# Kernel optimization log

Measured on AMD Instinct MI355X. Metric: run time of the kernel, lower is better.

The kernel has to match this reference:

```python
import jax, jax.numpy as jnp
import numpy as np

N, E, IN_DIM, OUT_DIM, H = 4096, 131072, 1024, 512, 4


def setup_inputs() -> dict:
    key = jax.random.key(0)
    k1, k2, k3, k4 = jax.random.split(key, 4)
    x = jax.random.normal(k1, (N, IN_DIM), dtype=jnp.float32)
    edge_index = jax.random.randint(k2, (2, E), 0, N, dtype=jnp.int64)
    # learned params, scaled like torch Linear init (~1/sqrt(fan_in))
    W = jax.random.normal(k3, (H, IN_DIM, OUT_DIM), dtype=jnp.float32) * 0.02
    a = jax.random.normal(k4, (H, 2 * OUT_DIM), dtype=jnp.float32) * 0.02
    return {"x": x, "edge_index": edge_index, "W": W, "a": a}


def reference(x, edge_index, W, a):
    row, col = edge_index[0], edge_index[1]
    n = x.shape[0]
    h = jnp.einsum('ni,hio->hno', x, W)                    # [H, N, out]
    # per-edge attention logits: a . [h[row] || h[col]]
    a_src, a_dst = a[:, :OUT_DIM], a[:, OUT_DIM:]
    e = (jnp.einsum('heo,ho->he', h[:, row], a_src)
         + jnp.einsum('heo,ho->he', h[:, col], a_dst))      # [H, E]
    e = jnp.where(e > 0, e, 0.2 * e)                        # LeakyReLU(0.2)
    # dense NxN attention matrix exactly as the original (zeros at non-edges
    # DO participate in the row softmax, matching the torch code)
    att = jnp.zeros((H, n, n), dtype=h.dtype).at[:, row, col].set(e)
    att = jax.nn.softmax(att, axis=-1)
    h_prime = jnp.einsum('hnm,hmo->hno', att, h)            # [H, N, out]
    return jnp.transpose(h_prime, (1, 0, 2)).reshape(n, H * OUT_DIM)
```

## Files before the change

### kernel.cpp

```cpp
#include <hip/hip_runtime.h>
#include <stdint.h>

#define NN 4096
#define EE 131072
#define IND 1024
#define OUTD 512
#define NH 4
#define NBKT 8
#define BKT_SHIFT 9

typedef __bf16 bf16x8 __attribute__((ext_vector_type(8)));
typedef float f32x4 __attribute__((ext_vector_type(4)));
typedef float f32x2 __attribute__((ext_vector_type(2)));

__device__ __forceinline__ unsigned short f2bf(float f) {
  unsigned u = __float_as_uint(f);
  u += 0x7FFFu + ((u >> 16) & 1u);
  return (unsigned short)(u >> 16);
}

__global__ void cast_x_kernel(const float* __restrict__ x, unsigned short* __restrict__ xb) {
  int i = blockIdx.x * 256 + threadIdx.x;
  float4 v = ((const float4*)x)[i];
  ushort4 o;
  o.x = f2bf(v.x); o.y = f2bf(v.y); o.z = f2bf(v.z); o.w = f2bf(v.w);
  ((ushort4*)xb)[i] = o;
}

__global__ void transpose_w_kernel(const float* __restrict__ W, unsigned short* __restrict__ Wt) {
  __shared__ float tile[32][33];
  int i0 = blockIdx.x * 32, o0 = blockIdx.y * 32, h = blockIdx.z;
  int tx = threadIdx.x, ty = threadIdx.y;
#pragma unroll
  for (int r = 0; r < 32; r += 8)
    tile[ty + r][tx] = W[((size_t)(h * IND + i0 + ty + r)) * OUTD + o0 + tx];
  __syncthreads();
#pragma unroll
  for (int r = 0; r < 32; r += 8)
    Wt[((size_t)(h * OUTD + o0 + ty + r)) * IND + i0 + tx] = f2bf(tile[tx][ty + r]);
}

__device__ __forceinline__ void gload16(const unsigned short* g, unsigned short* l) {
  __builtin_amdgcn_global_load_lds((const __attribute__((address_space(1))) void*)g,
                                   (__attribute__((address_space(3))) void*)l, 16, 0, 0);
}

__global__ __launch_bounds__(256, 2) void gemm_kernel(
    const unsigned short* __restrict__ X, const unsigned short* __restrict__ Wt,
    const float* __restrict__ Av, unsigned char* __restrict__ Hb8,
    float* __restrict__ s4_src, float* __restrict__ s4_dst, float* __restrict__ Scol) {
  __shared__ __align__(16) unsigned short As[2][4096];
  __shared__ __align__(16) unsigned short Bs[2][4096];
  const int t = threadIdx.x, w = t >> 6, lane = t & 63;
  const int bx = blockIdx.x, by = blockIdx.y, hh = blockIdx.z;

  const unsigned short* Ab0 = X + (size_t)(by * 128) * IND;
  const unsigned short* Bb0 = Wt + (size_t)(hh * OUTD + bx * 128) * IND;

  const int seg0 = w * 64 + lane, seg1 = (4 + w) * 64 + lane;
  const int r0 = seg0 >> 2, c0 = (seg0 & 3) ^ (r0 & 3);
  const int r1 = seg1 >> 2, c1 = (seg1 & 3) ^ (r1 & 3);

  const int wr = w >> 1, wc = w & 1, g = lane >> 4, rlo = lane & 15;
  int aoff[4], boff[4];
#pragma unroll
  for (int i = 0; i < 4; i++) {
    int ra = wr * 64 + i * 16 + rlo;
    aoff[i] = ra * 64 + ((g ^ (ra & 3)) << 4);
    int rb = wc * 64 + i * 16 + rlo;
    boff[i] = rb * 64 + ((g ^ (rb & 3)) << 4);
  }

  f32x4 zero = {0.f, 0.f, 0.f, 0.f};
  f32x4 acc[4][4];
#pragma unroll
  for (int i = 0; i < 4; i++)
#pragma unroll
    for (int j = 0; j < 4; j++) acc[i][j] = zero;

#define STAGE(buf, kt)                                                   \
  do {                                                                   \
    const unsigned short* ga = Ab0 + (kt) * 32;                          \
    const unsigned short* gb = Bb0 + (kt) * 32;                          \
    gload16(ga + r0 * IND + c0 * 8, &As[buf][w * 512]);                  \
    gload16(ga + r1 * IND + c1 * 8, &As[buf][(4 + w) * 512]);            \
    gload16(gb + r0 * IND + c0 * 8, &Bs[buf][w * 512]);                  \
    gload16(gb + r1 * IND + c1 * 8, &Bs[buf][(4 + w) * 512]);            \
  } while (0)

  STAGE(0, 0);
  __syncthreads();
  int cur = 0;
  for (int kt = 0; kt < 32; ++kt) {
    if (kt != 31) STAGE(cur ^ 1, kt + 1);
    const char* Abuf = (const char*)As[cur];
    const char* Bbuf = (const char*)Bs[cur];
    bf16x8 av[4], bv[4];
#pragma unroll
    for (int i = 0; i < 4; i++) {
      av[i] = *(const bf16x8*)(Abuf + aoff[i]);
      bv[i] = *(const bf16x8*)(Bbuf + boff[i]);
    }
#pragma unroll
    for (int i = 0; i < 4; i++)
#pragma unroll
      for (int j = 0; j < 4; j++)
        acc[i][j] = __builtin_amdgcn_mfma_f32_16x16x32_bf16(av[i], bv[j], acc[i][j], 0, 0, 0);
    __syncthreads();
    cur ^= 1;
  }
#undef STAGE

#pragma unroll
  for (int i = 0; i < 4; i++)
#pragma unroll
    for (int j = 0; j < 4; j++) {
      int mm0 = by * 128 + wr * 64 + i * 16 + g * 4;
      int nn = bx * 128 + wc * 64 + j * 16 + rlo;
#pragma unroll
      for (int q = 0; q < 4; q++) {
        int p = __builtin_amdgcn_cvt_pk_fp8_f32(acc[i][j][q], acc[i][j][q], 0, false);
        Hb8[((size_t)(mm0 + q) * NH + hh) * OUTD + nn] = (unsigned char)p;
      }
    }

  float as_[4], ad_[4];
#pragma unroll
  for (int j = 0; j < 4; j++) {
    int nn = bx * 128 + wc * 64 + j * 16 + rlo;
    as_[j] = Av[hh * 2 * OUTD + nn];
    ad_[j] = Av[hh * 2 * OUTD + OUTD + nn];
  }
#pragma unroll
  for (int i = 0; i < 4; i++)
#pragma unroll
    for (int q = 0; q < 4; q++) {
      float vs = 0.f, vd = 0.f;
#pragma unroll
      for (int j = 0; j < 4; j++) {
        float tv = acc[i][j][q];
        vs += tv * as_[j];
        vd += tv * ad_[j];
      }
#pragma unroll
      for (int m = 1; m < 16; m <<= 1) {
        vs += __shfl_xor(vs, m);
        vd += __shfl_xor(vd, m);
      }
      if (rlo == 0) {
        int r = by * 128 + wr * 64 + i * 16 + g * 4 + q;
        atomicAdd(&s4_src[r * NH + hh], vs);
        atomicAdd(&s4_dst[r * NH + hh], vd);
      }
    }

#pragma unroll
  for (int j = 0; j < 4; j++) {
    float cv = 0.f;
#pragma unroll
    for (int i = 0; i < 4; i++)
#pragma unroll
      for (int q = 0; q < 4; q++) cv += acc[i][j][q];
    cv += __shfl_xor(cv, 16);
    cv += __shfl_xor(cv, 32);
    if (g == 0) {
      int nn = bx * 128 + wc * 64 + j * 16 + rlo;
      atomicAdd(&Scol[hh * OUTD + nn], cv);
    }
  }
}

__global__ void edge_a_kernel(const int* __restrict__ ei, unsigned* __restrict__ bitmap,
                              int* __restrict__ counts2, unsigned char* __restrict__ flags) {
  int e = blockIdx.x * 256 + threadIdx.x;
  int row = ei[e], col = ei[EE + e];
  unsigned key = ((unsigned)row << 12) | (unsigned)col;
  unsigned bit = 1u << (key & 31);
  unsigned old = atomicOr(&bitmap[key >> 5], bit);
  if (old & bit) { flags[e] = 1; return; }
  flags[e] = 0;
  atomicAdd(&counts2[row * NBKT + (col >> BKT_SHIFT)], 1);
}

__global__ void scan_part_kernel(const int* __restrict__ counts2, int* __restrict__ bsum) {
  __shared__ int wsum[4];
  int b = blockIdx.x, t = threadIdx.x, w = t >> 6, lane = t & 63;
  int v = counts2[b * 256 + t];
#pragma unroll
  for (int d = 1; d < 64; d <<= 1) v += __shfl_xor(v, d);
  if (lane == 0) wsum[w] = v;
  __syncthreads();
  if (t == 0) bsum[b] = wsum[0] + wsum[1] + wsum[2] + wsum[3];
}

__global__ void scan_top_kernel(const int* __restrict__ bsum, int* __restrict__ bpre,
                                int* __restrict__ offsets2) {
  int t = threadIdx.x;
  int v0 = bsum[2 * t], v1 = bsum[2 * t + 1];
  int s = v0 + v1, inc = s;
#pragma unroll
  for (int d = 1; d < 64; d <<= 1) {
    int u = __shfl_up(inc, d);
    if (t >= d) inc += u;
  }
  int excl = inc - s;
  bpre[2 * t] = excl;
  bpre[2 * t + 1] = excl + v0;
  if (t == 63) offsets2[NN * NBKT] = inc;
}

__global__ void scan_down_kernel(const int* __restrict__ counts2, const int* __restrict__ bpre,
                                 int* __restrict__ offsets2, int* __restrict__ cursor2) {
  __shared__ int wsum[4];
  int b = blockIdx.x, t = threadIdx.x, w = t >> 6, lane = t & 63;
  int idx = b * 256 + t;
  int v = counts2[idx];
  int inc = v;
#pragma unroll
  for (int d = 1; d < 64; d <<= 1) {
    int u = __shfl_up(inc, d);
    if (lane >= d) inc += u;
  }
  if (lane == 63) wsum[w] = inc;
  __syncthreads();
  int wpre = 0;
#pragma unroll
  for (int k = 0; k < 4; k++)
    if (k < w) wpre += wsum[k];
  int excl = bpre[b] + wpre + inc - v;
  offsets2[idx] = excl;
  cursor2[idx] = excl;
}

__global__ void edge_b_kernel(const int* __restrict__ ei, const unsigned char* __restrict__ flags,
                              const float* __restrict__ s4_src, const float* __restrict__ s4_dst,
                              int* __restrict__ cursor2, int* __restrict__ csr_col,
                              float* __restrict__ csr_g4) {
  int e = blockIdx.x * 256 + threadIdx.x;
  if (flags[e]) return;
  int row = ei[e], col = ei[EE + e];
  int pos = atomicAdd(&cursor2[row * NBKT + (col >> BKT_SHIFT)], 1);
  csr_col[pos] = col;
  float4 ss = *(const float4*)(s4_src + row * NH);
  float4 sd = *(const float4*)(s4_dst + col * NH);
  float4 gv;
  float e0 = ss.x + sd.x; e0 = e0 > 0.f ? e0 : 0.2f * e0; gv.x = expf(e0) - 1.0f;
  float e1 = ss.y + sd.y; e1 = e1 > 0.f ? e1 : 0.2f * e1; gv.y = expf(e1) - 1.0f;
  float e2 = ss.z + sd.z; e2 = e2 > 0.f ? e2 : 0.2f * e2; gv.z = expf(e2) - 1.0f;
  float e3 = ss.w + sd.w; e3 = e3 > 0.f ? e3 : 0.2f * e3; gv.w = expf(e3) - 1.0f;
  *(float4*)(csr_g4 + (size_t)pos * NH) = gv;
}

__global__ __launch_bounds__(256) void finalize_kernel(
    const unsigned char* __restrict__ Hb8,
    const float* __restrict__ S, const int* __restrict__ offsets2,
    const int* __restrict__ csr_col, const float* __restrict__ csr_g4,
    float* __restrict__ out) {
  __shared__ int cols_s[64];
  __shared__ float g_s[4][64];
  const int i = blockIdx.x, t = threadIdx.x;
  const int w = t >> 6, lane = t & 63;

  float acc[8];
  {
    const float4* Sv = (const float4*)(S + w * OUTD + lane * 8);
    float4 s0 = Sv[0], s1 = Sv[1];
    acc[0] = s0.x; acc[1] = s0.y; acc[2] = s0.z; acc[3] = s0.w;
    acc[4] = s1.x; acc[5] = s1.y; acc[6] = s1.z; acc[7] = s1.w;
  }
  float gsum = 0.f;

  const int start = offsets2[i * NBKT];
  const int cnt = offsets2[(i + 1) * NBKT] - start;
  for (int base = 0; base < cnt; base += 64) {
    int nload = min(64, cnt - base);
    __syncthreads();
    if (w == 0) cols_s[lane] = (lane < nload) ? csr_col[start + base + lane] : 0;
    {
      int el = t >> 2;
      float gvv = (el < nload) ? csr_g4[(size_t)(start + base) * NH + t] : 0.f;
      g_s[t & 3][el] = gvv;
    }
    __syncthreads();
#pragma unroll 2
    for (int k = 0; k < nload; k++) {
      int cc = cols_s[k];
      float gg = g_s[w][k];
      gsum += gg;
      uint2 u = *(const uint2*)(Hb8 + ((size_t)(cc * NH + w)) * OUTD + lane * 8);
      f32x2 p0 = __builtin_amdgcn_cvt_pk_f32_fp8(u.x, false);
      f32x2 p1 = __builtin_amdgcn_cvt_pk_f32_fp8(u.x, true);
      f32x2 p2 = __builtin_amdgcn_cvt_pk_f32_fp8(u.y, false);
      f32x2 p3 = __builtin_amdgcn_cvt_pk_f32_fp8(u.y, true);
      acc[0] += gg * p0[0];
      acc[1] += gg * p0[1];
      acc[2] += gg * p1[0];
      acc[3] += gg * p1[1];
      acc[4] += gg * p2[0];
      acc[5] += gg * p2[1];
      acc[6] += gg * p3[0];
      acc[7] += gg * p3[1];
    }
  }

  float inv = 1.0f / ((float)NN + gsum);
  float4 o0, o1;
  o0.x = acc[0] * inv; o0.y = acc[1] * inv; o0.z = acc[2] * inv; o0.w = acc[3] * inv;
  o1.x = acc[4] * inv; o1.y = acc[5] * inv; o1.z = acc[6] * inv; o1.w = acc[7] * inv;
  float* ob = out + (size_t)i * (NH * OUTD) + w * OUTD + lane * 8;
  ((float4*)ob)[0] = o0;
  ((float4*)ob)[1] = o1;
}

extern "C" void kernel_launch(void* const* d_in, const int* in_sizes, int n_in,
                              void* d_out, int out_size, void* d_ws, size_t ws_size,
                              hipStream_t stream) {
  const float* x = (const float*)d_in[0];
  const int* ei = (const int*)d_in[1];
  const float* W = (const float*)d_in[2];
  const float* a = (const float*)d_in[3];
  float* out = (float*)d_out;

  char* ws = (char*)d_ws;
  unsigned short* xb = (unsigned short*)(ws);
  unsigned short* wt = (unsigned short*)(ws + (8ull << 20));
  unsigned char* Hb8 = (unsigned char*)(ws + (12ull << 20));
  char* scal = ws + (20ull << 20);
  float* s4_src = (float*)(scal);
  float* s4_dst = (float*)(scal + 65536);
  float* Scol = (float*)(scal + 2 * 65536);
  unsigned char* flags = (unsigned char*)(ws + (21ull << 20));
  unsigned* bitmap = (unsigned*)(ws + (22ull << 20));
  int* counts2 = (int*)(ws + (24ull << 20));
  int* offsets2 = (int*)(ws + (24ull << 20) + 262144);
  int* cursor2 = (int*)(ws + (24ull << 20) + 2 * 262144);
  int* bsum = (int*)(ws + (24ull << 20) + 3 * 262144);
  int* bpre = (int*)(ws + (24ull << 20) + 3 * 262144 + 1024);
  int* csr_col = (int*)(ws + (25ull << 20));
  float* csr_g4 = (float*)(ws + (26ull << 20));

  hipMemsetAsync(scal, 0, 2 * 65536 + 8192, stream);
  hipMemsetAsync(bitmap, 0, (size_t)NN * NN / 8, stream);
  hipMemsetAsync(counts2, 0, NN * NBKT * 4, stream);

  cast_x_kernel<<<4096, 256, 0, stream>>>(x, xb);
  transpose_w_kernel<<<dim3(32, 16, 4), dim3(32, 8), 0, stream>>>(W, wt);
  gemm_kernel<<<dim3(4, 32, 4), 256, 0, stream>>>(xb, wt, a, Hb8, s4_src, s4_dst, Scol);
  edge_a_kernel<<<EE / 256, 256, 0, stream>>>(ei, bitmap, counts2, flags);
  scan_part_kernel<<<128, 256, 0, stream>>>(counts2, bsum);
  scan_top_kernel<<<1, 64, 0, stream>>>(bsum, bpre, offsets2);
  scan_down_kernel<<<128, 256, 0, stream>>>(counts2, bpre, offsets2, cursor2);
  edge_b_kernel<<<EE / 256, 256, 0, stream>>>(ei, flags, s4_src, s4_dst, cursor2, csr_col,
                                              csr_g4);
  finalize_kernel<<<NN, 256, 0, stream>>>(Hb8, Scol, offsets2, csr_col, csr_g4, out);
}
```

Baseline: 184.1 us.

## Merge prep kernels, single-block scan, one memset, GEMM block swizzle, deeper unroll

Merges the x cast and W transpose into one launch and replaces the three-kernel scan with one 1024-thread block. The three memsets become one by placing the zeroed buffers next to each other. The GEMM grid is flattened into a 1D grid with a remapped block order to change how blocks land across XCDs and the cache, and the finalize inner loop is unrolled 4x instead of 2x. The main aim is fewer launches and less launch gap. The single-block scan runs serially over 32K counters, and the unroll may raise register pressure.

```diff
diff --git a/kernel.cpp b/kernel.cpp
--- a/kernel.cpp
+++ b/kernel.cpp
@@ -19,25 +19,28 @@
   return (unsigned short)(u >> 16);
 }
 
-__global__ void cast_x_kernel(const float* __restrict__ x, unsigned short* __restrict__ xb) {
-  int i = blockIdx.x * 256 + threadIdx.x;
-  float4 v = ((const float4*)x)[i];
-  ushort4 o;
-  o.x = f2bf(v.x); o.y = f2bf(v.y); o.z = f2bf(v.z); o.w = f2bf(v.w);
-  ((ushort4*)xb)[i] = o;
-}
-
-__global__ void transpose_w_kernel(const float* __restrict__ W, unsigned short* __restrict__ Wt) {
+__global__ void prep_kernel(const float* __restrict__ x, unsigned short* __restrict__ xb,
+                            const float* __restrict__ W, unsigned short* __restrict__ Wt) {
   __shared__ float tile[32][33];
-  int i0 = blockIdx.x * 32, o0 = blockIdx.y * 32, h = blockIdx.z;
-  int tx = threadIdx.x, ty = threadIdx.y;
-#pragma unroll
-  for (int r = 0; r < 32; r += 8)
-    tile[ty + r][tx] = W[((size_t)(h * IND + i0 + ty + r)) * OUTD + o0 + tx];
-  __syncthreads();
-#pragma unroll
-  for (int r = 0; r < 32; r += 8)
-    Wt[((size_t)(h * OUTD + o0 + ty + r)) * IND + i0 + tx] = f2bf(tile[tx][ty + r]);
+  const int bid = blockIdx.x, t = threadIdx.x;
+  if (bid < 4096) {
+    int i = bid * 256 + t;
+    float4 v = ((const float4*)x)[i];
+    ushort4 o;
+    o.x = f2bf(v.x); o.y = f2bf(v.y); o.z = f2bf(v.z); o.w = f2bf(v.w);
+    ((ushort4*)xb)[i] = o;
+  } else {
+    int b2 = bid - 4096;
+    int i0 = (b2 & 31) * 32, o0 = ((b2 >> 5) & 15) * 32, h = b2 >> 9;
+    int tx = t & 31, ty = t >> 5;
+#pragma unroll
+    for (int r = 0; r < 32; r += 8)
+      tile[ty + r][tx] = W[((size_t)(h * IND + i0 + ty + r)) * OUTD + o0 + tx];
+    __syncthreads();
+#pragma unroll
+    for (int r = 0; r < 32; r += 8)
+      Wt[((size_t)(h * OUTD + o0 + ty + r)) * IND + i0 + tx] = f2bf(tile[tx][ty + r]);
+  }
 }
 
 __device__ __forceinline__ void gload16(const unsigned short* g, unsigned short* l) {
@@ -52,7 +55,9 @@
   __shared__ __align__(16) unsigned short As[2][4096];
   __shared__ __align__(16) unsigned short Bs[2][4096];
   const int t = threadIdx.x, w = t >> 6, lane = t & 63;
-  const int bx = blockIdx.x, by = blockIdx.y, hh = blockIdx.z;
+  const int B = blockIdx.x;
+  const int L = ((B & 7) << 6) | (B >> 3);
+  const int bx = L & 3, hh = (L >> 2) & 3, by = L >> 4;
 
   const unsigned short* Ab0 = X + (size_t)(by * 128) * IND;
   const unsigned short* Bb0 = Wt + (size_t)(hh * OUTD + bx * 128) * IND;
@@ -182,54 +187,46 @@
   atomicAdd(&counts2[row * NBKT + (col >> BKT_SHIFT)], 1);
 }
 
-__global__ void scan_part_kernel(const int* __restrict__ counts2, int* __restrict__ bsum) {
-  __shared__ int wsum[4];
-  int b = blockIdx.x, t = threadIdx.x, w = t >> 6, lane = t & 63;
-  int v = counts2[b * 256 + t];
-#pragma unroll
-  for (int d = 1; d < 64; d <<= 1) v += __shfl_xor(v, d);
-  if (lane == 0) wsum[w] = v;
-  __syncthreads();
-  if (t == 0) bsum[b] = wsum[0] + wsum[1] + wsum[2] + wsum[3];
-}
-
-__global__ void scan_top_kernel(const int* __restrict__ bsum, int* __restrict__ bpre,
-                                int* __restrict__ offsets2) {
-  int t = threadIdx.x;
-  int v0 = bsum[2 * t], v1 = bsum[2 * t + 1];
-  int s = v0 + v1, inc = s;
-#pragma unroll
-  for (int d = 1; d < 64; d <<= 1) {
-    int u = __shfl_up(inc, d);
-    if (t >= d) inc += u;
-  }
-  int excl = inc - s;
-  bpre[2 * t] = excl;
-  bpre[2 * t + 1] = excl + v0;
-  if (t == 63) offsets2[NN * NBKT] = inc;
-}
-
-__global__ void scan_down_kernel(const int* __restrict__ counts2, const int* __restrict__ bpre,
-                                 int* __restrict__ offsets2, int* __restrict__ cursor2) {
-  __shared__ int wsum[4];
-  int b = blockIdx.x, t = threadIdx.x, w = t >> 6, lane = t & 63;
-  int idx = b * 256 + t;
-  int v = counts2[idx];
-  int inc = v;
+__global__ __launch_bounds__(1024) void scan_kernel(const int* __restrict__ c2,
+                                                    int* __restrict__ off2,
+                                                    int* __restrict__ cur2) {
+  __shared__ int wtot[16];
+  const int t = threadIdx.x, w = t >> 6, lane = t & 63;
+  int loc[32];
+  const int4* src = (const int4*)c2 + t * 8;
+#pragma unroll
+  for (int k = 0; k < 8; k++) {
+    int4 v = src[k];
+    loc[4 * k] = v.x; loc[4 * k + 1] = v.y; loc[4 * k + 2] = v.z; loc[4 * k + 3] = v.w;
+  }
+  int s = 0;
+#pragma unroll
+  for (int k = 0; k < 32; k++) s += loc[k];
+  int inc = s;
 #pragma unroll
   for (int d = 1; d < 64; d <<= 1) {
     int u = __shfl_up(inc, d);
     if (lane >= d) inc += u;
   }
-  if (lane == 63) wsum[w] = inc;
+  if (lane == 63) wtot[w] = inc;
   __syncthreads();
   int wpre = 0;
-#pragma unroll
-  for (int k = 0; k < 4; k++)
-    if (k < w) wpre += wsum[k];
-  int excl = bpre[b] + wpre + inc - v;
-  offsets2[idx] = excl;
-  cursor2[idx] = excl;
+  for (int k = 0; k < 16; k++)
+    if (k < w) wpre += wtot[k];
+  int o = wpre + inc - s;
+  if (t == 1023) off2[NN * NBKT] = o + s;
+  int4* od = (int4*)off2 + t * 8;
+  int4* cd = (int4*)cur2 + t * 8;
+#pragma unroll
+  for (int k = 0; k < 8; k++) {
+    int4 ov;
+    ov.x = o; o += loc[4 * k];
+    ov.y = o; o += loc[4 * k + 1];
+    ov.z = o; o += loc[4 * k + 2];
+    ov.w = o; o += loc[4 * k + 3];
+    od[k] = ov;
+    cd[k] = ov;
+  }
 }
 
 __global__ void edge_b_kernel(const int* __restrict__ ei, const unsigned char* __restrict__ flags,
@@ -282,7 +279,7 @@
       g_s[t & 3][el] = gvv;
     }
     __syncthreads();
-#pragma unroll 2
+#pragma unroll 4
     for (int k = 0; k < nload; k++) {
       int cc = cols_s[k];
       float gg = g_s[w][k];
@@ -325,31 +322,25 @@
   unsigned short* xb = (unsigned short*)(ws);
   unsigned short* wt = (unsigned short*)(ws + (8ull << 20));
   unsigned char* Hb8 = (unsigned char*)(ws + (12ull << 20));
-  char* scal = ws + (20ull << 20);
-  float* s4_src = (float*)(scal);
-  float* s4_dst = (float*)(scal + 65536);
-  float* Scol = (float*)(scal + 2 * 65536);
-  unsigned char* flags = (unsigned char*)(ws + (21ull << 20));
-  unsigned* bitmap = (unsigned*)(ws + (22ull << 20));
-  int* counts2 = (int*)(ws + (24ull << 20));
-  int* offsets2 = (int*)(ws + (24ull << 20) + 262144);
-  int* cursor2 = (int*)(ws + (24ull << 20) + 2 * 262144);
-  int* bsum = (int*)(ws + (24ull << 20) + 3 * 262144);
-  int* bpre = (int*)(ws + (24ull << 20) + 3 * 262144 + 1024);
-  int* csr_col = (int*)(ws + (25ull << 20));
-  float* csr_g4 = (float*)(ws + (26ull << 20));
-
-  hipMemsetAsync(scal, 0, 2 * 65536 + 8192, stream);
-  hipMemsetAsync(bitmap, 0, (size_t)NN * NN / 8, stream);
-  hipMemsetAsync(counts2, 0, NN * NBKT * 4, stream);
-
-  cast_x_kernel<<<4096, 256, 0, stream>>>(x, xb);
-  transpose_w_kernel<<<dim3(32, 16, 4), dim3(32, 8), 0, stream>>>(W, wt);
-  gemm_kernel<<<dim3(4, 32, 4), 256, 0, stream>>>(xb, wt, a, Hb8, s4_src, s4_dst, Scol);
+  char* zreg = ws + (20ull << 20);
+  float* s4_src = (float*)(zreg);
+  float* s4_dst = (float*)(zreg + 65536);
+  float* Scol = (float*)(zreg + 2 * 65536);
+  int* counts2 = (int*)(zreg + 2 * 65536 + 8192);
+  unsigned* bitmap = (unsigned*)(zreg + 2 * 65536 + 8192 + 131072);
+  const size_t ZBYTES = 2 * 65536 + 8192 + 131072 + ((size_t)NN * NN / 8);
+  unsigned char* flags = (unsigned char*)(ws + (23ull << 20));
+  int* offsets2 = (int*)(ws + (23ull << 20) + 262144);
+  int* cursor2 = (int*)(ws + (23ull << 20) + 2 * 262144);
+  int* csr_col = (int*)(ws + (24ull << 20));
+  float* csr_g4 = (float*)(ws + (25ull << 20));
+
+  hipMemsetAsync(zreg, 0, ZBYTES, stream);
+
+  prep_kernel<<<4096 + 2048, 256, 0, stream>>>(x, xb, W, wt);
+  gemm_kernel<<<512, 256, 0, stream>>>(xb, wt, a, Hb8, s4_src, s4_dst, Scol);
   edge_a_kernel<<<EE / 256, 256, 0, stream>>>(ei, bitmap, counts2, flags);
-  scan_part_kernel<<<128, 256, 0, stream>>>(counts2, bsum);
-  scan_top_kernel<<<1, 64, 0, stream>>>(bsum, bpre, offsets2);
-  scan_down_kernel<<<128, 256, 0, stream>>>(counts2, bpre, offsets2, cursor2);
+  scan_kernel<<<1, 1024, 0, stream>>>(counts2, offsets2, cursor2);
   edge_b_kernel<<<EE / 256, 256, 0, stream>>>(ei, flags, s4_src, s4_dst, cursor2, csr_col,
                                               csr_g4);
   finalize_kernel<<<NN, 256, 0, stream>>>(Hb8, Scol, offsets2, csr_col, csr_g4, out);
```

Measured after the change: 192.7 us. 4.7% more time.
